# Kernel optimization log

Measured on AMD Instinct MI355X. Metric: run time of the kernel, lower is better.

The kernel has to match this reference:

```python
import jax, jax.numpy as jnp
import numpy as np

HEADS = 8
EPS_BN = 1e-5
EPS_L2 = 1e-12


def _conv(x, w, b=None, pad=0, groups=1):
    out = jax.lax.conv_general_dilated(
        x, w, (1, 1), [(pad, pad), (pad, pad)],
        feature_group_count=groups,
        dimension_numbers=('NCHW', 'OIHW', 'NCHW'))
    if b is not None:
        out = out + b[None, :, None, None]
    return out


def _sobel_weight(in_ch):
    # Fixed (non-trainable) Sobel kernels, exactly as built in SobelConv2d.__init__
    w = np.zeros((4, in_ch, 3, 3), np.float32)
    for idx in range(4):
        if idx % 2 == 0:
            w[idx, :, 0, :] = -1; w[idx, :, 0, 1] = -2
            w[idx, :, -1, :] = 1; w[idx, :, -1, 1] = 2
        else:
            w[idx, :, :, 0] = -1; w[idx, :, 1, 0] = -2
            w[idx, :, :, -1] = 1; w[idx, :, 1, -1] = 2
    return jnp.asarray(w)


def _l2norm(t):
    # F.normalize(p=2, dim=-1): x / clamp_min(||x||, eps)
    n = jnp.linalg.norm(t, axis=-1, keepdims=True)
    return t / jnp.maximum(n, EPS_L2)


def _forward(x_in, SAR_img, Wq, Wk, Wv, rescale, Wp, bp, pe1_w, pe2_w,
             conv3_w, conv3_b, bn_g, bn_b, sobel_b,
             conv2_w, conv2_b, conv32_w, conv32_b, dconv_w, dconv_b):
    b, h, w, c = x_in.shape
    d = c // HEADS
    n = h * w

    # --- SAR-guided mask (SARGuidedMechanism.forward) ---
    a = _conv(SAR_img, conv3_w, conv3_b, pad=1)
    # BatchNorm2d in training mode: batch statistics over (N,H,W)
    mu = a.mean(axis=(0, 2, 3), keepdims=True)
    var = a.var(axis=(0, 2, 3), keepdims=True)
    bn = (a - mu) / jnp.sqrt(var + EPS_BN) * bn_g[None, :, None, None] + bn_b[None, :, None, None]
    s = _conv(bn, _sobel_weight(SAR_img.shape[1]), sobel_b, pad=1)  # [b,4,H,W]
    sob = jnp.stack([jnp.sqrt(s[:, 0] ** 2 + s[:, 1] ** 2),
                     jnp.sqrt(s[:, 2] ** 2 + s[:, 3] ** 2)], axis=1)  # [b,2,H,W]
    sar_sobel = sob + bn
    e1 = _conv(sar_sobel, conv2_w, conv2_b)                           # 1x1 conv -> [b,c,H,W]
    e2 = jax.nn.sigmoid(_conv(sar_sobel, conv32_w, conv32_b, pad=1))
    e3 = _conv(e1, dconv_w, dconv_b, pad=2, groups=c)                 # depth_conv(conv2(.)) == depthwise(e1)
    mask = (e1 + e2 + e3).transpose(0, 2, 3, 1).reshape(b, n, c)      # [b,n,c]

    # --- channel (transposed) attention ---
    x = x_in.reshape(b, n, c)
    q_inp = x @ Wq
    k_inp = x @ Wk
    v_inp = x @ Wv

    def split(t):  # [b,n,(heads d)] -> [b,heads,d,n]
        return t.reshape(b, n, HEADS, d).transpose(0, 2, 3, 1)

    q = _l2norm(split(q_inp))          # normalize over token axis n
    k = _l2norm(split(k_inp))
    v = split(v_inp * mask)            # SAR gate fused into V

    attn = jnp.einsum('bhin,bhjn->bhij', k, q) * rescale[None]        # [b,heads,d,d]
    attn = jax.nn.softmax(attn, axis=-1)
    o = jnp.einsum('bhij,bhjn->bhin', attn, v)                        # [b,heads,d,n]
    o = o.transpose(0, 3, 1, 2).reshape(b, n, c)
    out_c = (o @ Wp + bp).reshape(b, h, w, c)

    # --- positional branch: depthwise conv -> GELU -> depthwise conv on v_inp ---
    vim = v_inp.reshape(b, h, w, c).transpose(0, 3, 1, 2)
    pe = _conv(vim, pe1_w, pad=1, groups=c)
    pe = jax.nn.gelu(pe, approximate=False)
    pe = _conv(pe, pe2_w, pad=1, groups=c).transpose(0, 2, 3, 1)

    return out_c + pe


def setup_inputs() -> dict:
    key = jax.random.key(0)
    ks = jax.random.split(key, 12)
    b, H, W, C, CS = 1, 256, 256, 512, 2
    wgt = lambda k, shp, sc=0.05: jax.random.normal(k, shp, jnp.float32) * sc
    return {
        'x_in': jax.random.normal(ks[0], (b, H, W, C), jnp.float32),
        'SAR_img': jax.random.normal(ks[1], (b, CS, H, W), jnp.float32),
        'Wq': wgt(ks[2], (C, C)),
        'Wk': wgt(ks[3], (C, C)),
        'Wv': wgt(ks[4], (C, C)),
        'rescale': jnp.ones((HEADS, 1, 1), jnp.float32),
        'Wp': wgt(ks[5], (C, C)),
        'bp': jnp.zeros((C,), jnp.float32),
        'pe1_w': wgt(ks[6], (C, 1, 3, 3), 0.1),
        'pe2_w': wgt(ks[7], (C, 1, 3, 3), 0.1),
        'conv3_w': wgt(ks[8], (CS, CS, 3, 3), 0.2),
        'conv3_b': jnp.zeros((CS,), jnp.float32),
        'bn_g': jnp.ones((CS,), jnp.float32),
        'bn_b': jnp.zeros((CS,), jnp.float32),
        'sobel_b': jnp.zeros((4,), jnp.float32),
        'conv2_w': wgt(ks[9], (C, CS, 1, 1), 0.1),
        'conv2_b': jnp.zeros((C,), jnp.float32),
        'conv32_w': wgt(ks[10], (C, CS, 3, 3), 0.1),
        'conv32_b': jnp.zeros((C,), jnp.float32),
        'dconv_w': wgt(ks[11], (C, 1, 5, 5), 0.1),
        'dconv_b': jnp.zeros((C,), jnp.float32),
    }


def reference(x_in, SAR_img, Wq, Wk, Wv, rescale, Wp, bp, pe1_w, pe2_w,
              conv3_w, conv3_b, bn_g, bn_b, sobel_b,
              conv2_w, conv2_b, conv32_w, conv32_b, dconv_w, dconv_b):
    return _forward(x_in, SAR_img, Wq, Wk, Wv, rescale, Wp, bp, pe1_w, pe2_w,
                    conv3_w, conv3_b, bn_g, bn_b, sobel_b,
                    conv2_w, conv2_b, conv32_w, conv32_b, dconv_w, dconv_b)
```

## Files before the change

### kernel.cpp

```cpp
#include <hip/hip_runtime.h>
#include <cstdint>
#include <cstdio>

typedef unsigned short u16;
typedef __attribute__((ext_vector_type(8))) short short8;
typedef __attribute__((ext_vector_type(4))) float f32x4;

#define DEVFN __device__ __forceinline__

DEVFN u16 f2bf(float f){ union{float f; unsigned u;} v; v.f=f; unsigned r = v.u + 0x7fffu + ((v.u>>16)&1u); return (u16)(r>>16); }
DEVFN float bf2f(u16 h){ union{unsigned u; float f;} v; v.u = ((unsigned)h)<<16; return v.f; }

#define GLOAD_LDS16(gp, lp) __builtin_amdgcn_global_load_lds( \
    (const __attribute__((address_space(1))) void*)(gp), \
    (__attribute__((address_space(3))) void*)(lp), 16, 0, 0)

static constexpr int NTOK = 65536;
static constexpr int GSPLIT = 32;
static constexpr int GKLEN  = NTOK / GSPLIT;

static constexpr size_t MB = 1024 * 1024;
static constexpr size_t OFF_XB    = 0;
static constexpr size_t OFF_XBT   = 64 * MB;
static constexpr size_t OFF_VB    = 128 * MB;
static constexpr size_t OFF_VT    = 192 * MB;
static constexpr size_t OFF_GPART = 256 * MB;
static constexpr size_t OFF_G     = 288 * MB;
static constexpr size_t OFF_TQ    = 289 * MB;
static constexpr size_t OFF_TK    = 290 * MB;
static constexpr size_t OFF_WVT   = 291 * MB;
static constexpr size_t OFF_W2T   = 291 * MB + 524288;
static constexpr size_t OFF_ASAR  = 292 * MB;
static constexpr size_t OFF_SS    = 292 * MB + 524288;
static constexpr size_t OFF_BNP   = 293 * MB;
static constexpr size_t OFF_QN    = 293 * MB + 4096;
static constexpr size_t OFF_KN    = 293 * MB + 8192;
static constexpr size_t OFF_ATTN  = 293 * MB + 12288;
static constexpr size_t WS_NEEDED = 294 * MB;

template<int MODE>
__global__ __launch_bounds__(256) void gemm_bt(
    const u16* __restrict__ A, int lda,
    const u16* __restrict__ B, int ldb,
    int klen,
    void* __restrict__ Cout,
    const float* __restrict__ bias)
{
  __shared__ uint4 smem[1024];
  const int tid  = threadIdx.x;
  const int lane = tid & 63;
  const int wv   = tid >> 6;
  const int wm   = (wv >> 1) * 64;
  const int wn   = (wv & 1) * 64;
  const int m0   = blockIdx.x * 128;
  const int n0   = blockIdx.y * 128;
  const int kb   = blockIdx.z * klen;

  const int q0 = tid, q1 = tid + 256;
  const size_t arow0 = (size_t)(m0 + (q0 >> 2)) * lda + (q0 & 3) * 8;
  const size_t arow1 = (size_t)(m0 + (q1 >> 2)) * lda + (q1 & 3) * 8;
  const size_t brow0 = (size_t)(n0 + (q0 >> 2)) * ldb + (q0 & 3) * 8;
  const size_t brow1 = (size_t)(n0 + (q1 >> 2)) * ldb + (q1 & 3) * 8;

  f32x4 acc[4][4] = {};
  const char* lAc = (const char*)smem;
  const char* lBc = (const char*)(smem + 512);
  const int ko = (lane >> 4) * 16;
  const int ma = lane & 15;

  for (int k0 = kb; k0 < kb + klen; k0 += 32) {
    __syncthreads();
    GLOAD_LDS16(&A[arow0 + k0], &smem[q0]);
    GLOAD_LDS16(&A[arow1 + k0], &smem[q1]);
    GLOAD_LDS16(&B[brow0 + k0], &smem[512 + q0]);
    GLOAD_LDS16(&B[brow1 + k0], &smem[512 + q1]);
    __syncthreads();
    short8 af[4], bfr[4];
#pragma unroll
    for (int mt = 0; mt < 4; mt++)
      af[mt] = *(const short8*)(lAc + (wm + mt * 16 + ma) * 64 + ko);
#pragma unroll
    for (int nt = 0; nt < 4; nt++)
      bfr[nt] = *(const short8*)(lBc + (wn + nt * 16 + ma) * 64 + ko);
#pragma unroll
    for (int mt = 0; mt < 4; mt++)
#pragma unroll
      for (int nt = 0; nt < 4; nt++)
        acc[mt][nt] = __builtin_amdgcn_mfma_f32_16x16x32_bf16(af[mt], bfr[nt], acc[mt][nt], 0, 0, 0);
  }

  const int col = lane & 15;
  const int rq  = (lane >> 4) * 4;
  float* Cf = (float*)Cout;
  u16*   Ch = (u16*)Cout;
  if (MODE == 1) Cf += (size_t)blockIdx.z * 512 * 512;
#pragma unroll
  for (int mt = 0; mt < 4; mt++) {
#pragma unroll
    for (int nt = 0; nt < 4; nt++) {
      const int mbase = m0 + wm + mt * 16 + rq;
      const int nn    = n0 + wn + nt * 16 + col;
#pragma unroll
      for (int r = 0; r < 4; r++) {
        float vv = acc[mt][nt][r];
        size_t idx = (size_t)(mbase + r) * 512 + nn;
        if (MODE == 0)      Ch[idx] = f2bf(vv);
        else if (MODE == 1) Cf[idx] = vv;
        else                Cf[idx] = vv + bias[nn];
      }
    }
  }
}

__global__ void k_cast_transpose(const float* __restrict__ x, u16* __restrict__ xb, u16* __restrict__ xbT)
{
  __shared__ u16 tile[64][72];
  const int t0 = blockIdx.x * 64, c0 = blockIdx.y * 64;
  const int tx = threadIdx.x & 15, ty = threadIdx.x >> 4;
#pragma unroll
  for (int p = 0; p < 4; p++) {
    int t = ty + p * 16;
    float4 v = *(const float4*)&x[(size_t)(t0 + t) * 512 + c0 + tx * 4];
    ushort4 u; u.x = f2bf(v.x); u.y = f2bf(v.y); u.z = f2bf(v.z); u.w = f2bf(v.w);
    *(ushort4*)&xb[(size_t)(t0 + t) * 512 + c0 + tx * 4] = u;
    tile[t][tx*4+0] = u.x; tile[t][tx*4+1] = u.y; tile[t][tx*4+2] = u.z; tile[t][tx*4+3] = u.w;
  }
  __syncthreads();
#pragma unroll
  for (int p = 0; p < 4; p++) {
    int c = ty + p * 16;
    ushort4 u;
    u.x = tile[tx*4+0][c]; u.y = tile[tx*4+1][c]; u.z = tile[tx*4+2][c]; u.w = tile[tx*4+3][c];
    *(ushort4*)&xbT[(size_t)(c0 + c) * 65536 + t0 + tx * 4] = u;
  }
}

__global__ void k_tbf16(const u16* __restrict__ src, u16* __restrict__ dst, int srows, int scols)
{
  __shared__ u16 tile[64][72];
  const int r0 = blockIdx.x * 64, c0v = blockIdx.y * 64;
  const int tx = threadIdx.x & 15, ty = threadIdx.x >> 4;
#pragma unroll
  for (int p = 0; p < 4; p++) {
    int r = ty + p * 16;
    ushort4 u = *(const ushort4*)&src[(size_t)(r0 + r) * scols + c0v + tx * 4];
    tile[r][tx*4+0] = u.x; tile[r][tx*4+1] = u.y; tile[r][tx*4+2] = u.z; tile[r][tx*4+3] = u.w;
  }
  __syncthreads();
#pragma unroll
  for (int p = 0; p < 4; p++) {
    int c = ty + p * 16;
    ushort4 u;
    u.x = tile[tx*4+0][c]; u.y = tile[tx*4+1][c]; u.z = tile[tx*4+2][c]; u.w = tile[tx*4+3][c];
    *(ushort4*)&dst[(size_t)(c0v + c) * srows + r0 + tx * 4] = u;
  }
}

__global__ void k_transpose_w(const float* __restrict__ Wsrc, u16* __restrict__ WT)
{
  __shared__ u16 tile[64][72];
  const int k0 = blockIdx.x * 64, n0 = blockIdx.y * 64;
  const int tx = threadIdx.x & 15, ty = threadIdx.x >> 4;
#pragma unroll
  for (int p = 0; p < 4; p++) {
    int t = ty + p * 16;
    float4 v = *(const float4*)&Wsrc[(size_t)(k0 + t) * 512 + n0 + tx * 4];
    tile[t][tx*4+0] = f2bf(v.x); tile[t][tx*4+1] = f2bf(v.y);
    tile[t][tx*4+2] = f2bf(v.z); tile[t][tx*4+3] = f2bf(v.w);
  }
  __syncthreads();
#pragma unroll
  for (int p = 0; p < 4; p++) {
    int c = ty + p * 16;
    ushort4 u;
    u.x = tile[tx*4+0][c]; u.y = tile[tx*4+1][c]; u.z = tile[tx*4+2][c]; u.w = tile[tx*4+3][c];
    *(ushort4*)&WT[(size_t)(n0 + c) * 512 + k0 + tx * 4] = u;
  }
}

__global__ void k_reduce_g(const float* __restrict__ part, float* __restrict__ G)
{
  const int i = blockIdx.x * 256 + threadIdx.x;
  float s = 0.f;
  for (int z = 0; z < GSPLIT; z++) s += part[(size_t)z * 262144 + i];
  G[i] = s;
}

__global__ __launch_bounds__(256) void k_gw(const float* __restrict__ G,
    const float* __restrict__ Wq, const float* __restrict__ Wk,
    float* __restrict__ Tq, float* __restrict__ Tk)
{
  const float* Bm = blockIdx.z ? Wk : Wq;
  float* Cm = blockIdx.z ? Tk : Tq;
  __shared__ float As[64][68];
  __shared__ float Bs[64][68];
  const int i0 = blockIdx.x * 64, j0 = blockIdx.y * 64;
  const int tx = threadIdx.x & 15, ty = threadIdx.x >> 4;
  float acc[4][4] = {};
  for (int k0 = 0; k0 < 512; k0 += 64) {
    __syncthreads();
#pragma unroll
    for (int p = 0; p < 4; p++) {
      int r = ty + p * 16;
      float4 a = *(const float4*)&G [(size_t)(i0 + r) * 512 + k0 + tx * 4];
      float4 b = *(const float4*)&Bm[(size_t)(k0 + r) * 512 + j0 + tx * 4];
      *(float4*)&As[r][tx * 4] = a;
      *(float4*)&Bs[r][tx * 4] = b;
    }
    __syncthreads();
    for (int kk = 0; kk < 64; kk++) {
      float a0 = As[ty*4+0][kk], a1 = As[ty*4+1][kk], a2 = As[ty*4+2][kk], a3 = As[ty*4+3][kk];
      float4 bq = *(const float4*)&Bs[kk][tx * 4];
      acc[0][0] += a0*bq.x; acc[0][1] += a0*bq.y; acc[0][2] += a0*bq.z; acc[0][3] += a0*bq.w;
      acc[1][0] += a1*bq.x; acc[1][1] += a1*bq.y; acc[1][2] += a1*bq.z; acc[1][3] += a1*bq.w;
      acc[2][0] += a2*bq.x; acc[2][1] += a2*bq.y; acc[2][2] += a2*bq.z; acc[2][3] += a2*bq.w;
      acc[3][0] += a3*bq.x; acc[3][1] += a3*bq.y; acc[3][2] += a3*bq.z; acc[3][3] += a3*bq.w;
    }
  }
#pragma unroll
  for (int u = 0; u < 4; u++) {
    float4 o = make_float4(acc[u][0], acc[u][1], acc[u][2], acc[u][3]);
    *(float4*)&Cm[(size_t)(i0 + ty * 4 + u) * 512 + j0 + tx * 4] = o;
  }
}

__global__ void k_norms(const float* __restrict__ Wq, const float* __restrict__ Tq,
                        const float* __restrict__ Wk, const float* __restrict__ Tk,
                        float* __restrict__ qn, float* __restrict__ kn)
{
  const int gw = (blockIdx.x * 256 + threadIdx.x) >> 6;
  const int lane = threadIdx.x & 63;
  const float* Wm = (gw < 512) ? Wq : Wk;
  const float* Tm = (gw < 512) ? Tq : Tk;
  const int c = gw & 511;
  float s = 0.f;
  for (int r = lane; r < 512; r += 64) s += Wm[(size_t)r * 512 + c] * Tm[(size_t)r * 512 + c];
  for (int off = 32; off > 0; off >>= 1) s += __shfl_down(s, off);
  if (lane == 0) {
    float n = sqrtf(fmaxf(s, 0.f));
    ((gw < 512) ? qn : kn)[c] = fmaxf(n, 1e-12f);
  }
}

__global__ __launch_bounds__(256) void k_attn(const float* __restrict__ Wk, const float* __restrict__ Tq,
    const float* __restrict__ qn, const float* __restrict__ kn,
    const float* __restrict__ rescale, float* __restrict__ attn)
{
  const int h = blockIdx.x, hd = h * 64;
  __shared__ float Ks[64][68];
  __shared__ float Qs[64][68];
  __shared__ float Ss[64][65];
  const int tx = threadIdx.x & 15, ty = threadIdx.x >> 4;
  float acc[4][4] = {};
  for (int k0 = 0; k0 < 512; k0 += 64) {
    __syncthreads();
#pragma unroll
    for (int p = 0; p < 4; p++) {
      int r = ty + p * 16;
      float4 a = *(const float4*)&Wk[(size_t)(k0 + r) * 512 + hd + tx * 4];
      float4 b = *(const float4*)&Tq[(size_t)(k0 + r) * 512 + hd + tx * 4];
      *(float4*)&Ks[r][tx * 4] = a;
      *(float4*)&Qs[r][tx * 4] = b;
    }
    __syncthreads();
    for (int kk = 0; kk < 64; kk++) {
      float a0 = Ks[kk][ty*4+0], a1 = Ks[kk][ty*4+1], a2 = Ks[kk][ty*4+2], a3 = Ks[kk][ty*4+3];
      float4 bq = *(const float4*)&Qs[kk][tx * 4];
      acc[0][0] += a0*bq.x; acc[0][1] += a0*bq.y; acc[0][2] += a0*bq.z; acc[0][3] += a0*bq.w;
      acc[1][0] += a1*bq.x; acc[1][1] += a1*bq.y; acc[1][2] += a1*bq.z; acc[1][3] += a1*bq.w;
      acc[2][0] += a2*bq.x; acc[2][1] += a2*bq.y; acc[2][2] += a2*bq.z; acc[2][3] += a2*bq.w;
      acc[3][0] += a3*bq.x; acc[3][1] += a3*bq.y; acc[3][2] += a3*bq.z; acc[3][3] += a3*bq.w;
    }
  }
#pragma unroll
  for (int u = 0; u < 4; u++)
#pragma unroll
    for (int v = 0; v < 4; v++)
      Ss[ty * 4 + u][tx * 4 + v] = acc[u][v];
  __syncthreads();
  if (threadIdx.x < 64) {
    const int i = threadIdx.x;
    const float sci = rescale[h] / kn[hd + i];
    float mx = -1e30f;
    for (int j = 0; j < 64; j++) {
      float L = Ss[i][j] * sci / qn[hd + j];
      Ss[i][j] = L;
      mx = fmaxf(mx, L);
    }
    float sum = 0.f;
    for (int j = 0; j < 64; j++) { float e = __expf(Ss[i][j] - mx); Ss[i][j] = e; sum += e; }
    float inv = 1.f / sum;
    for (int j = 0; j < 64; j++) attn[(size_t)h * 4096 + i * 64 + j] = Ss[i][j] * inv;
  }
}

__global__ void k_w2t(const float* __restrict__ attn, const float* __restrict__ Wp, u16* __restrict__ W2T)
{
  const int h = blockIdx.x >> 3, e0 = (blockIdx.x & 7) * 64;
  __shared__ float As[64][65];
  for (int p = 0; p < 16; p++) {
    int idx = p * 256 + threadIdx.x;
    As[idx >> 6][idx & 63] = attn[(size_t)h * 4096 + idx];
  }
  __syncthreads();
  const int e = e0 + (threadIdx.x & 63);
  const int j4 = threadIdx.x >> 6;
  float s[16];
#pragma unroll
  for (int jj = 0; jj < 16; jj++) s[jj] = 0.f;
  for (int i = 0; i < 64; i++) {
    float wv_ = Wp[(size_t)(h * 64 + i) * 512 + e];
#pragma unroll
    for (int jj = 0; jj < 16; jj++) s[jj] += As[i][j4 * 16 + jj] * wv_;
  }
#pragma unroll
  for (int jj = 0; jj < 16; jj++)
    W2T[(size_t)e * 512 + h * 64 + j4 * 16 + jj] = f2bf(s[jj]);
}

__global__ void k_conv3(const float* __restrict__ sar, const float* __restrict__ w3,
                        const float* __restrict__ b3, float* __restrict__ a)
{
  const int oc = blockIdx.y;
  const int p = blockIdx.x * 256 + threadIdx.x;
  const int y = p >> 8, x = p & 255;
  float s = b3[oc];
#pragma unroll
  for (int ic = 0; ic < 2; ic++) {
    const float* img = sar + ic * 65536;
    const float* w = w3 + oc * 18 + ic * 9;
#pragma unroll
    for (int k = 0; k < 9; k++) {
      int yy = y + k / 3 - 1, xx = x + k % 3 - 1;
      if ((unsigned)yy < 256u && (unsigned)xx < 256u) s += w[k] * img[yy * 256 + xx];
    }
  }
  a[oc * 65536 + p] = s;
}

__global__ void k_bnstats(const float* __restrict__ a, const float* __restrict__ g,
                          const float* __restrict__ b, float* __restrict__ bnp)
{
  const int ch = blockIdx.x;
  const int tid = threadIdx.x;
  const float* src = a + ch * 65536;
  float s = 0.f, sq = 0.f;
  for (int i = tid; i < 65536; i += 256) { float v = src[i]; s += v; sq += v * v; }
  __shared__ float rs[256], rq[256];
  rs[tid] = s; rq[tid] = sq;
  __syncthreads();
  for (int o = 128; o > 0; o >>= 1) {
    if (tid < o) { rs[tid] += rs[tid + o]; rq[tid] += rq[tid + o]; }
    __syncthreads();
  }
  if (tid == 0) {
    float mu = rs[0] * (1.f / 65536.f);
    float var = rq[0] * (1.f / 65536.f) - mu * mu;
    float scale = g[ch] / sqrtf(var + 1e-5f);
    bnp[ch] = scale;
    bnp[2 + ch] = b[ch] - mu * scale;
  }
}

__global__ void k_sar2(const float* __restrict__ a, const float* __restrict__ bnp,
                       const float* __restrict__ sb, float* __restrict__ ss)
{
  const int p = blockIdx.x * 256 + threadIdx.x;
  const int y = p >> 8, x = p & 255;
  const float sc0 = bnp[0], sc1 = bnp[1], sh0 = bnp[2], sh1 = bnp[3];
  float bs[9];
  float bn0c = 0.f, bn1c = 0.f;
#pragma unroll
  for (int k = 0; k < 9; k++) {
    int yy = y + k / 3 - 1, xx = x + k % 3 - 1;
    float v0 = 0.f, v1 = 0.f;
    if ((unsigned)yy < 256u && (unsigned)xx < 256u) {
      int q = yy * 256 + xx;
      v0 = a[q] * sc0 + sh0;
      v1 = a[65536 + q] * sc1 + sh1;
    }
    bs[k] = v0 + v1;
    if (k == 4) { bn0c = v0; bn1c = v1; }
  }
  float gv = (bs[6] + 2.f * bs[7] + bs[8]) - (bs[0] + 2.f * bs[1] + bs[2]);
  float gh = (bs[2] + 2.f * bs[5] + bs[8]) - (bs[0] + 2.f * bs[3] + bs[6]);
  float s0 = gv + sb[0], s1 = gh + sb[1], s2 = gv + sb[2], s3 = gh + sb[3];
  ss[p]         = sqrtf(s0 * s0 + s1 * s1) + bn0c;
  ss[65536 + p] = sqrtf(s2 * s2 + s3 * s3) + bn1c;
}

__global__ __launch_bounds__(256) void k_mask2(
    const float* __restrict__ ss,
    const float* __restrict__ w2,  const float* __restrict__ b2,
    const float* __restrict__ w32, const float* __restrict__ b32,
    const float* __restrict__ dw,  const float* __restrict__ db,
    const u16* __restrict__ vt, u16* __restrict__ vmt)
{
  __shared__ __align__(16) float sw0[1296];
  __shared__ __align__(16) float sw1[1296];
  __shared__ __align__(16) float swi[1296];
  const int bxx = blockIdx.x & 7, byy = blockIdx.x >> 3;
  const int tx0 = bxx * 32, ty0 = byy * 32;
  const int c0 = blockIdx.y * 4;
  const bool border = (bxx == 0) || (bxx == 7) || (byy == 0) || (byy == 7);

  for (int i = threadIdx.x; i < 1296; i += 256) {
    int r = i / 36, cl = i - r * 36;
    int gy = ty0 - 2 + r, gx = tx0 - 2 + cl;
    bool in = ((unsigned)gy < 256u) & ((unsigned)gx < 256u);
    int gp = gy * 256 + gx;
    sw0[i] = in ? ss[gp] : 0.f;
    sw1[i] = in ? ss[65536 + gp] : 0.f;
    swi[i] = in ? 1.f : 0.f;
  }
  __syncthreads();

  const int g = threadIdx.x & 7;
  const int row = threadIdx.x >> 3;
  float u0[4][4] = {}, u1[4][4] = {}, ui[4][4] = {}, a32[4][4] = {};
  float s0c[4], s1c[4];

#pragma unroll
  for (int ky = 0; ky < 5; ky++) {
    const float* rp0 = &sw0[(row + ky) * 36 + g * 4];
    const float* rp1 = &sw1[(row + ky) * 36 + g * 4];
    float4 p0a = *(const float4*)rp0, p0b = *(const float4*)(rp0 + 4);
    float4 p1a = *(const float4*)rp1, p1b = *(const float4*)(rp1 + 4);
    float r0[8] = {p0a.x, p0a.y, p0a.z, p0a.w, p0b.x, p0b.y, p0b.z, p0b.w};
    float r1[8] = {p1a.x, p1a.y, p1a.z, p1a.w, p1b.x, p1b.y, p1b.z, p1b.w};
    if (ky == 2) {
#pragma unroll
      for (int j = 0; j < 4; j++) { s0c[j] = r0[j + 2]; s1c[j] = r1[j + 2]; }
    }
#pragma unroll
    for (int dx = 0; dx < 5; dx++) {
#pragma unroll
      for (int cc = 0; cc < 4; cc++) {
        float wdw = dw[(c0 + cc) * 25 + ky * 5 + dx];
#pragma unroll
        for (int j = 0; j < 4; j++) {
          u0[cc][j] += wdw * r0[dx + j];
          u1[cc][j] += wdw * r1[dx + j];
        }
      }
    }
    if (border) {
      const float* rpi = &swi[(row + ky) * 36 + g * 4];
      float4 pia = *(const float4*)rpi, pib = *(const float4*)(rpi + 4);
      float ri[8] = {pia.x, pia.y, pia.z, pia.w, pib.x, pib.y, pib.z, pib.w};
#pragma unroll
      for (int dx = 0; dx < 5; dx++)
#pragma unroll
        for (int cc = 0; cc < 4; cc++) {
          float wdw = dw[(c0 + cc) * 25 + ky * 5 + dx];
#pragma unroll
          for (int j = 0; j < 4; j++) ui[cc][j] += wdw * ri[dx + j];
        }
    }
    if (ky >= 1 && ky <= 3) {
#pragma unroll
      for (int dx = 0; dx < 3; dx++)
#pragma unroll
        for (int cc = 0; cc < 4; cc++) {
          float wa = w32[(c0 + cc) * 18 + (ky - 1) * 3 + dx];
          float wb = w32[(c0 + cc) * 18 + 9 + (ky - 1) * 3 + dx];
#pragma unroll
          for (int j = 0; j < 4; j++)
            a32[cc][j] += wa * r0[dx + 1 + j] + wb * r1[dx + 1 + j];
        }
    }
  }

  const int y = ty0 + row, xg = tx0 + g * 4;
#pragma unroll
  for (int cc = 0; cc < 4; cc++) {
    const int c = c0 + cc;
    const float a = w2[c * 2], b = w2[c * 2 + 1], beta = b2[c];
    const float bb = b32[c], dbv = db[c];
    float wsum = 0.f;
    if (!border) {
#pragma unroll
      for (int t = 0; t < 25; t++) wsum += dw[c * 25 + t];
    }
    ushort4 vv = *(const ushort4*)&vt[(size_t)c * 65536 + y * 256 + xg];
    float vf[4] = {bf2f(vv.x), bf2f(vv.y), bf2f(vv.z), bf2f(vv.w)};
    ushort4 o;
    u16 ov[4];
#pragma unroll
    for (int j = 0; j < 4; j++) {
      float W = border ? ui[cc][j] : wsum;
      float sig = 1.f / (1.f + __expf(-(a32[cc][j] + bb)));
      float m = a * (s0c[j] + u0[cc][j]) + b * (s1c[j] + u1[cc][j])
              + beta * (1.f + W) + sig + dbv;
      ov[j] = f2bf(vf[j] * m);
    }
    o.x = ov[0]; o.y = ov[1]; o.z = ov[2]; o.w = ov[3];
    *(ushort4*)&vmt[(size_t)c * 65536 + y * 256 + xg] = o;
  }
}

DEVFN void dw3x3_row4(const u16* plane, int y, int x0, int sub,
                      const float* w9, float& s0, float& s1, float& s2, float& s3)
{
#pragma unroll
  for (int r = 0; r < 3; r++) {
    int yy = y + r - 1;
    if ((unsigned)yy < 256u) {
      const int base = yy * 256 + x0 + sub * 4;
      ushort4 p = *(const ushort4*)&plane[base];
      float v0 = bf2f(p.x), v1 = bf2f(p.y), v2 = bf2f(p.z), v3 = bf2f(p.w);
      float lf = __shfl_up(v3, 1);
      float rt = __shfl_down(v0, 1);
      if (sub == 0)  lf = (x0 > 0)   ? bf2f(plane[yy * 256 + x0 - 1])  : 0.f;
      if (sub == 15) rt = (x0 < 192) ? bf2f(plane[yy * 256 + x0 + 64]) : 0.f;
      const float wa = w9[r * 3], wb = w9[r * 3 + 1], wc = w9[r * 3 + 2];
      s0 += wa * lf + wb * v0 + wc * v1;
      s1 += wa * v0 + wb * v1 + wc * v2;
      s2 += wa * v1 + wb * v2 + wc * v3;
      s3 += wa * v2 + wb * v3 + wc * rt;
    }
  }
}

__global__ __launch_bounds__(256) void k_pe1v(const u16* __restrict__ vt,
    const float* __restrict__ w, u16* __restrict__ gt)
{
  const int t = blockIdx.x;
  const int y = t >> 2, x0 = (t & 3) * 64;
  const int cg = blockIdx.y * 64;
  const int lane = threadIdx.x & 63, wvq = threadIdx.x >> 6;
  const int sub = lane & 15, chq = lane >> 4;
#pragma unroll
  for (int i = 0; i < 4; i++) {
    const int c = cg + wvq * 16 + i * 4 + chq;
    const u16* plane = vt + (size_t)c * 65536;
    float w9[9];
#pragma unroll
    for (int k = 0; k < 9; k++) w9[k] = w[c * 9 + k];
    float s0 = 0.f, s1 = 0.f, s2 = 0.f, s3 = 0.f;
    dw3x3_row4(plane, y, x0, sub, w9, s0, s1, s2, s3);
    const float ksc = 0.70710678118654752f;
    s0 = 0.5f * s0 * (1.f + erff(s0 * ksc));
    s1 = 0.5f * s1 * (1.f + erff(s1 * ksc));
    s2 = 0.5f * s2 * (1.f + erff(s2 * ksc));
    s3 = 0.5f * s3 * (1.f + erff(s3 * ksc));
    ushort4 o; o.x = f2bf(s0); o.y = f2bf(s1); o.z = f2bf(s2); o.w = f2bf(s3);
    *(ushort4*)&gt[(size_t)c * 65536 + y * 256 + x0 + sub * 4] = o;
  }
}

__global__ __launch_bounds__(256) void k_pe2v(const u16* __restrict__ gt,
    const float* __restrict__ w, float* __restrict__ out)
{
  __shared__ float tile[64][65];
  const int t = blockIdx.x;
  const int y = t >> 2, x0 = (t & 3) * 64;
  const int cg = blockIdx.y * 64;
  const int lane = threadIdx.x & 63, wvq = threadIdx.x >> 6;
  const int sub = lane & 15, chq = lane >> 4;
#pragma unroll
  for (int i = 0; i < 4; i++) {
    const int cl = wvq * 16 + i * 4 + chq;
    const int c = cg + cl;
    const u16* plane = gt + (size_t)c * 65536;
    float w9[9];
#pragma unroll
    for (int k = 0; k < 9; k++) w9[k] = w[c * 9 + k];
    float s0 = 0.f, s1 = 0.f, s2 = 0.f, s3 = 0.f;
    dw3x3_row4(plane, y, x0, sub, w9, s0, s1, s2, s3);
    tile[cl][sub * 4 + 0] = s0;
    tile[cl][sub * 4 + 1] = s1;
    tile[cl][sub * 4 + 2] = s2;
    tile[cl][sub * 4 + 3] = s3;
  }
  __syncthreads();
#pragma unroll
  for (int k = 0; k < 4; k++) {
    const int idx = k * 256 + threadIdx.x;
    const int q = idx & 15, pl = idx >> 4;
    float4 add = make_float4(tile[q * 4 + 0][pl], tile[q * 4 + 1][pl],
                             tile[q * 4 + 2][pl], tile[q * 4 + 3][pl]);
    float* op = &out[(size_t)(y * 256 + x0 + pl) * 512 + cg + q * 4];
    float4 o = *(float4*)op;
    o.x += add.x; o.y += add.y; o.z += add.z; o.w += add.w;
    *(float4*)op = o;
  }
}

extern "C" void kernel_launch(void* const* d_in, const int* in_sizes, int n_in,
                              void* d_out, int out_size, void* d_ws, size_t ws_size,
                              hipStream_t stream)
{
  (void)in_sizes; (void)n_in; (void)out_size;
  const float* x    = (const float*)d_in[0];
  const float* sar  = (const float*)d_in[1];
  const float* Wq   = (const float*)d_in[2];
  const float* Wk   = (const float*)d_in[3];
  const float* Wv   = (const float*)d_in[4];
  const float* resc = (const float*)d_in[5];
  const float* Wp   = (const float*)d_in[6];
  const float* bp   = (const float*)d_in[7];
  const float* pe1w = (const float*)d_in[8];
  const float* pe2w = (const float*)d_in[9];
  const float* w3   = (const float*)d_in[10];
  const float* b3   = (const float*)d_in[11];
  const float* bng  = (const float*)d_in[12];
  const float* bnb  = (const float*)d_in[13];
  const float* sb   = (const float*)d_in[14];
  const float* w2c  = (const float*)d_in[15];
  const float* b2c  = (const float*)d_in[16];
  const float* w32  = (const float*)d_in[17];
  const float* b32  = (const float*)d_in[18];
  const float* dw   = (const float*)d_in[19];
  const float* db   = (const float*)d_in[20];
  float* out = (float*)d_out;

  if (ws_size < WS_NEEDED)
    fprintf(stderr, "MS_MSA: workspace too small: have %zu need %zu\n", ws_size, WS_NEEDED);

  char* ws = (char*)d_ws;
  u16* XB    = (u16*)(ws + OFF_XB);
  u16* XBT   = (u16*)(ws + OFF_XBT);
  u16* VB    = (u16*)(ws + OFF_VB);
  u16* VT    = (u16*)(ws + OFF_VT);
  float* GPART = (float*)(ws + OFF_GPART);
  float* G     = (float*)(ws + OFF_G);
  float* TQ    = (float*)(ws + OFF_TQ);
  float* TK    = (float*)(ws + OFF_TK);
  u16* WVT   = (u16*)(ws + OFF_WVT);
  u16* W2T   = (u16*)(ws + OFF_W2T);
  float* ASAR = (float*)(ws + OFF_ASAR);
  float* SS   = (float*)(ws + OFF_SS);
  float* BNP  = (float*)(ws + OFF_BNP);
  float* QN   = (float*)(ws + OFF_QN);
  float* KN   = (float*)(ws + OFF_KN);
  float* ATTN = (float*)(ws + OFF_ATTN);
  u16* VMT = XB;
  u16* GT  = XBT;
  u16* VM  = VB;

  k_cast_transpose<<<dim3(1024, 8), 256, 0, stream>>>(x, XB, XBT);
  gemm_bt<1><<<dim3(4, 4, GSPLIT), 256, 0, stream>>>(XBT, NTOK, XBT, NTOK, GKLEN, GPART, nullptr);
  k_reduce_g<<<1024, 256, 0, stream>>>(GPART, G);
  k_transpose_w<<<dim3(8, 8), 256, 0, stream>>>(Wv, WVT);
  gemm_bt<0><<<dim3(512, 4), 256, 0, stream>>>(XB, 512, WVT, 512, 512, VB, nullptr);
  k_tbf16<<<dim3(1024, 8), 256, 0, stream>>>(VB, VT, 65536, 512);
  k_gw<<<dim3(8, 8, 2), 256, 0, stream>>>(G, Wq, Wk, TQ, TK);
  k_norms<<<256, 256, 0, stream>>>(Wq, TQ, Wk, TK, QN, KN);
  k_attn<<<8, 256, 0, stream>>>(Wk, TQ, QN, KN, resc, ATTN);
  k_w2t<<<64, 256, 0, stream>>>(ATTN, Wp, W2T);
  k_conv3<<<dim3(256, 2), 256, 0, stream>>>(sar, w3, b3, ASAR);
  k_bnstats<<<2, 256, 0, stream>>>(ASAR, bng, bnb, BNP);
  k_sar2<<<256, 256, 0, stream>>>(ASAR, BNP, sb, SS);
  k_mask2<<<dim3(64, 128), 256, 0, stream>>>(SS, w2c, b2c, w32, b32, dw, db, VT, VMT);
  k_tbf16<<<dim3(8, 1024), 256, 0, stream>>>(VMT, VM, 512, 65536);
  gemm_bt<2><<<dim3(512, 4), 256, 0, stream>>>(VM, 512, W2T, 512, 512, out, bp);
  k_pe1v<<<dim3(1024, 8), 256, 0, stream>>>(VT, pe1w, GT);
  k_pe2v<<<dim3(1024, 8), 256, 0, stream>>>(GT, pe2w, out);
}
```

Baseline: 977.4 us.

## Recast SAR mask convolutions as bf16 split-precision MFMA GEMM over im2col patches

```diff
diff --git a/kernel.cpp b/kernel.cpp
--- a/kernel.cpp
+++ b/kernel.cpp
@@ -36,6 +36,8 @@
 static constexpr size_t OFF_QN    = 293 * MB + 4096;
 static constexpr size_t OFF_KN    = 293 * MB + 8192;
 static constexpr size_t OFF_ATTN  = 293 * MB + 12288;
+static constexpr size_t OFF_BM    = 293 * MB + 262144;
+static constexpr size_t OFF_TB    = 293 * MB + 786432;
 static constexpr size_t WS_NEEDED = 294 * MB;
 
 template<int MODE>
@@ -389,113 +391,196 @@
   ss[65536 + p] = sqrtf(s2 * s2 + s3 * s3) + bn1c;
 }
 
-__global__ __launch_bounds__(256) void k_mask2(
-    const float* __restrict__ ss,
-    const float* __restrict__ w2,  const float* __restrict__ b2,
-    const float* __restrict__ w32, const float* __restrict__ b32,
-    const float* __restrict__ dw,  const float* __restrict__ db,
-    const u16* __restrict__ vt, u16* __restrict__ vmt)
-{
-  __shared__ __align__(16) float sw0[1296];
-  __shared__ __align__(16) float sw1[1296];
-  __shared__ __align__(16) float swi[1296];
-  const int bxx = blockIdx.x & 7, byy = blockIdx.x >> 3;
-  const int tx0 = bxx * 32, ty0 = byy * 32;
-  const int c0 = blockIdx.y * 4;
-  const bool border = (bxx == 0) || (bxx == 7) || (byy == 0) || (byy == 7);
-
-  for (int i = threadIdx.x; i < 1296; i += 256) {
-    int r = i / 36, cl = i - r * 36;
-    int gy = ty0 - 2 + r, gx = tx0 - 2 + cl;
-    bool in = ((unsigned)gy < 256u) & ((unsigned)gx < 256u);
-    int gp = gy * 256 + gx;
-    sw0[i] = in ? ss[gp] : 0.f;
-    sw1[i] = in ? ss[65536 + gp] : 0.f;
-    swi[i] = in ? 1.f : 0.f;
+
+__global__ void k_dwprep(const float* __restrict__ dw, const float* __restrict__ db,
+                         const float* __restrict__ w2, const float* __restrict__ b2,
+                         const float* __restrict__ w32, const float* __restrict__ b32,
+                         u16* __restrict__ BM, float* __restrict__ TB)
+{
+  const int c = blockIdx.x * 256 + threadIdx.x;
+  if (c >= 512) return;
+  float d[25];
+  float wsum = 0.f;
+#pragma unroll
+  for (int t = 0; t < 25; t++) { d[t] = dw[c * 25 + t]; wsum += d[t]; }
+  const float a = w2[2 * c], b = w2[2 * c + 1], beta = b2[c];
+  const float C1 = beta * (1.f + wsum) + db[c];
+
+  u16* rL1 = BM + (size_t)((c >> 6) * 128 + (c & 63)) * 192;
+  u16* rL2 = rL1 + (size_t)64 * 192;
+
+#pragma unroll
+  for (int k = 0; k < 64; k++) {
+    float v1;
+    if (k < 25)       v1 = a * (d[k] + (k == 12 ? 1.f : 0.f));
+    else if (k < 50)  v1 = b * (d[k - 25] + (k == 37 ? 1.f : 0.f));
+    else if (k == 63) v1 = C1;
+    else              v1 = 0.f;
+    u16 h = f2bf(v1); u16 l = f2bf(v1 - bf2f(h));
+    rL1[k] = h; rL1[64 + k] = h; rL1[128 + k] = l;
+  }
+#pragma unroll
+  for (int k = 0; k < 64; k++) {
+    float v2 = 0.f;
+    if (k < 50) {
+      const int t = (k < 25) ? k : (k - 25);
+      const int dy = t / 5 - 2, dx = t % 5 - 2;
+      if (dy >= -1 && dy <= 1 && dx >= -1 && dx <= 1)
+        v2 = w32[c * 18 + ((k < 25) ? 0 : 9) + (dy + 1) * 3 + (dx + 1)];
+    }
+    if (k == 63) v2 = b32[c];
+    u16 h = f2bf(v2); u16 l = f2bf(v2 - bf2f(h));
+    rL2[k] = h; rL2[64 + k] = h; rL2[128 + k] = l;
+  }
+
+  float rs[5], cs[5];
+#pragma unroll
+  for (int i = 0; i < 5; i++) {
+    rs[i] = d[i*5] + d[i*5+1] + d[i*5+2] + d[i*5+3] + d[i*5+4];
+    cs[i] = d[i] + d[5+i] + d[10+i] + d[15+i] + d[20+i];
+  }
+  float* tb = TB + (size_t)c * 32;
+  tb[0] = rs[0];  tb[1] = rs[0] + rs[1];
+  tb[2] = rs[4];  tb[3] = rs[3] + rs[4];
+  tb[4] = cs[0];  tb[5] = cs[0] + cs[1];
+  tb[6] = cs[4];  tb[7] = cs[3] + cs[4];
+  tb[8]  = d[0];           tb[9]  = d[0] + d[1];
+  tb[10] = d[0] + d[5];    tb[11] = d[0] + d[1] + d[5] + d[6];
+  tb[12] = d[4];           tb[13] = d[3] + d[4];
+  tb[14] = d[4] + d[9];    tb[15] = d[3] + d[4] + d[8] + d[9];
+  tb[16] = d[20];          tb[17] = d[20] + d[21];
+  tb[18] = d[15] + d[20];  tb[19] = d[15] + d[16] + d[20] + d[21];
+  tb[20] = d[24];          tb[21] = d[23] + d[24];
+  tb[22] = d[19] + d[24];  tb[23] = d[18] + d[19] + d[23] + d[24];
+#pragma unroll
+  for (int i = 24; i < 32; i++) tb[i] = 0.f;
+}
+
+__global__ __launch_bounds__(256) void k_patch(const float* __restrict__ ss, u16* __restrict__ P)
+{
+  __shared__ float s0r[5][264];
+  __shared__ float s1r[5][264];
+  const int y = blockIdx.x;
+  const int tid = threadIdx.x;
+  for (int i = tid; i < 1300; i += 256) {
+    const int r = i / 260, col = i - r * 260;
+    const int yy = y + r - 2, xx = col - 2;
+    const bool in = ((unsigned)yy < 256u) & ((unsigned)xx < 256u);
+    const int gp = yy * 256 + xx;
+    s0r[r][col] = in ? ss[gp] : 0.f;
+    s1r[r][col] = in ? ss[65536 + gp] : 0.f;
   }
   __syncthreads();
-
-  const int g = threadIdx.x & 7;
-  const int row = threadIdx.x >> 3;
-  float u0[4][4] = {}, u1[4][4] = {}, ui[4][4] = {}, a32[4][4] = {};
-  float s0c[4], s1c[4];
-
-#pragma unroll
-  for (int ky = 0; ky < 5; ky++) {
-    const float* rp0 = &sw0[(row + ky) * 36 + g * 4];
-    const float* rp1 = &sw1[(row + ky) * 36 + g * 4];
-    float4 p0a = *(const float4*)rp0, p0b = *(const float4*)(rp0 + 4);
-    float4 p1a = *(const float4*)rp1, p1b = *(const float4*)(rp1 + 4);
-    float r0[8] = {p0a.x, p0a.y, p0a.z, p0a.w, p0b.x, p0b.y, p0b.z, p0b.w};
-    float r1[8] = {p1a.x, p1a.y, p1a.z, p1a.w, p1b.x, p1b.y, p1b.z, p1b.w};
-    if (ky == 2) {
-#pragma unroll
-      for (int j = 0; j < 4; j++) { s0c[j] = r0[j + 2]; s1c[j] = r1[j + 2]; }
-    }
+  const int x = tid;
+  unsigned arr32[64];
+#pragma unroll
+  for (int i = 0; i < 64; i++) arr32[i] = 0u;
+#define PUTK(k, v) arr32[(k) >> 1] |= ((unsigned)(v)) << (((k) & 1) * 16)
+#pragma unroll
+  for (int dy = 0; dy < 5; dy++)
 #pragma unroll
     for (int dx = 0; dx < 5; dx++) {
-#pragma unroll
-      for (int cc = 0; cc < 4; cc++) {
-        float wdw = dw[(c0 + cc) * 25 + ky * 5 + dx];
-#pragma unroll
-        for (int j = 0; j < 4; j++) {
-          u0[cc][j] += wdw * r0[dx + j];
-          u1[cc][j] += wdw * r1[dx + j];
+      const int t = dy * 5 + dx;
+      const float v0 = s0r[dy][x + dx];
+      const float v1 = s1r[dy][x + dx];
+      const u16 h0 = f2bf(v0); const u16 l0 = f2bf(v0 - bf2f(h0));
+      const u16 h1 = f2bf(v1); const u16 l1 = f2bf(v1 - bf2f(h1));
+      PUTK(t, h0);      PUTK(25 + t, h1);
+      PUTK(64 + t, l0); PUTK(89 + t, l1);
+    }
+  PUTK(63, 0x3F80u);
+#undef PUTK
+  unsigned* dst = (unsigned*)(P + (size_t)(y * 256 + x) * 192);
+#pragma unroll
+  for (int i = 0; i < 16; i++)
+    *(uint4*)(dst + i * 4) = *(const uint4*)(arr32 + i * 4);
+#pragma unroll
+  for (int i = 0; i < 8; i++)
+    *(uint4*)(dst + 64 + i * 4) = *(const uint4*)(arr32 + i * 4);
+}
+
+__global__ __launch_bounds__(256) void k_maskmm(
+    const u16* __restrict__ P, const u16* __restrict__ BM,
+    const float* __restrict__ TB, const float* __restrict__ beta_p,
+    u16* __restrict__ VB)
+{
+  __shared__ uint4 smem[1024];
+  const int tid  = threadIdx.x;
+  const int lane = tid & 63;
+  const int wv   = tid >> 6;
+  const int m0   = blockIdx.x * 128;
+  const int g    = blockIdx.y;
+
+  const int q0 = tid, q1 = tid + 256;
+  const size_t arow0 = (size_t)(m0 + (q0 >> 2)) * 192 + (q0 & 3) * 8;
+  const size_t arow1 = (size_t)(m0 + (q1 >> 2)) * 192 + (q1 & 3) * 8;
+  const size_t brow0 = (size_t)(g * 128 + (q0 >> 2)) * 192 + (q0 & 3) * 8;
+  const size_t brow1 = (size_t)(g * 128 + (q1 >> 2)) * 192 + (q1 & 3) * 8;
+
+  f32x4 acc[2][8] = {};
+  const char* lAc = (const char*)smem;
+  const char* lBc = (const char*)(smem + 512);
+  const int ko = (lane >> 4) * 16;
+  const int ma = lane & 15;
+
+  for (int k0 = 0; k0 < 192; k0 += 32) {
+    __syncthreads();
+    GLOAD_LDS16(&P[arow0 + k0],  &smem[q0]);
+    GLOAD_LDS16(&P[arow1 + k0],  &smem[q1]);
+    GLOAD_LDS16(&BM[brow0 + k0], &smem[512 + q0]);
+    GLOAD_LDS16(&BM[brow1 + k0], &smem[512 + q1]);
+    __syncthreads();
+    short8 af[2], bfr[8];
+#pragma unroll
+    for (int mt = 0; mt < 2; mt++)
+      af[mt] = *(const short8*)(lAc + (wv * 32 + mt * 16 + ma) * 64 + ko);
+#pragma unroll
+    for (int nt = 0; nt < 8; nt++)
+      bfr[nt] = *(const short8*)(lBc + (nt * 16 + ma) * 64 + ko);
+#pragma unroll
+    for (int mt = 0; mt < 2; mt++)
+#pragma unroll
+      for (int nt = 0; nt < 8; nt++)
+        acc[mt][nt] = __builtin_amdgcn_mfma_f32_16x16x32_bf16(af[mt], bfr[nt], acc[mt][nt], 0, 0, 0);
+  }
+
+  const int col = lane & 15, rq = (lane >> 4) * 4;
+  const int y   = m0 >> 8;
+  const int mty = (y < 2) ? (2 - y) : 0;
+  const int mby = (y > 253) ? (y - 253) : 0;
+#pragma unroll
+  for (int mt = 0; mt < 2; mt++) {
+#pragma unroll
+    for (int nt = 0; nt < 4; nt++) {
+      const int ch = g * 64 + nt * 16 + col;
+#pragma unroll
+      for (int r = 0; r < 4; r++) {
+        const int px = m0 + wv * 32 + mt * 16 + rq + r;
+        const float L1 = acc[mt][nt][r];
+        const float L2 = acc[mt][nt + 4][r];
+        const int x  = px & 255;
+        const int ml = (x < 2) ? (2 - x) : 0;
+        const int mr = (x > 253) ? (x - 253) : 0;
+        float wc = 0.f;
+        if (mty | mby | ml | mr) {
+          const float* tb = &TB[(size_t)ch * 32];
+          float W = 0.f;
+          if (mty) W -= tb[mty - 1];
+          if (mby) W -= tb[2 + mby - 1];
+          if (ml)  W -= tb[4 + ml - 1];
+          if (mr)  W -= tb[6 + mr - 1];
+          if (mty && ml) W += tb[8  + (mty - 1) * 2 + (ml - 1)];
+          if (mty && mr) W += tb[12 + (mty - 1) * 2 + (mr - 1)];
+          if (mby && ml) W += tb[16 + (mby - 1) * 2 + (ml - 1)];
+          if (mby && mr) W += tb[20 + (mby - 1) * 2 + (mr - 1)];
+          wc = beta_p[ch] * W;
         }
+        const float sig  = 1.f / (1.f + __expf(-L2));
+        const float mask = L1 + wc + sig;
+        const size_t idx = (size_t)px * 512 + ch;
+        VB[idx] = f2bf(bf2f(VB[idx]) * mask);
       }
     }
-    if (border) {
-      const float* rpi = &swi[(row + ky) * 36 + g * 4];
-      float4 pia = *(const float4*)rpi, pib = *(const float4*)(rpi + 4);
-      float ri[8] = {pia.x, pia.y, pia.z, pia.w, pib.x, pib.y, pib.z, pib.w};
-#pragma unroll
-      for (int dx = 0; dx < 5; dx++)
-#pragma unroll
-        for (int cc = 0; cc < 4; cc++) {
-          float wdw = dw[(c0 + cc) * 25 + ky * 5 + dx];
-#pragma unroll
-          for (int j = 0; j < 4; j++) ui[cc][j] += wdw * ri[dx + j];
-        }
-    }
-    if (ky >= 1 && ky <= 3) {
-#pragma unroll
-      for (int dx = 0; dx < 3; dx++)
-#pragma unroll
-        for (int cc = 0; cc < 4; cc++) {
-          float wa = w32[(c0 + cc) * 18 + (ky - 1) * 3 + dx];
-          float wb = w32[(c0 + cc) * 18 + 9 + (ky - 1) * 3 + dx];
-#pragma unroll
-          for (int j = 0; j < 4; j++)
-            a32[cc][j] += wa * r0[dx + 1 + j] + wb * r1[dx + 1 + j];
-        }
-    }
-  }
-
-  const int y = ty0 + row, xg = tx0 + g * 4;
-#pragma unroll
-  for (int cc = 0; cc < 4; cc++) {
-    const int c = c0 + cc;
-    const float a = w2[c * 2], b = w2[c * 2 + 1], beta = b2[c];
-    const float bb = b32[c], dbv = db[c];
-    float wsum = 0.f;
-    if (!border) {
-#pragma unroll
-      for (int t = 0; t < 25; t++) wsum += dw[c * 25 + t];
-    }
-    ushort4 vv = *(const ushort4*)&vt[(size_t)c * 65536 + y * 256 + xg];
-    float vf[4] = {bf2f(vv.x), bf2f(vv.y), bf2f(vv.z), bf2f(vv.w)};
-    ushort4 o;
-    u16 ov[4];
-#pragma unroll
-    for (int j = 0; j < 4; j++) {
-      float W = border ? ui[cc][j] : wsum;
-      float sig = 1.f / (1.f + __expf(-(a32[cc][j] + bb)));
-      float m = a * (s0c[j] + u0[cc][j]) + b * (s1c[j] + u1[cc][j])
-              + beta * (1.f + W) + sig + dbv;
-      ov[j] = f2bf(vf[j] * m);
-    }
-    o.x = ov[0]; o.y = ov[1]; o.z = ov[2]; o.w = ov[3];
-    *(ushort4*)&vmt[(size_t)c * 65536 + y * 256 + xg] = o;
   }
 }
 
@@ -635,9 +720,10 @@
   float* QN   = (float*)(ws + OFF_QN);
   float* KN   = (float*)(ws + OFF_KN);
   float* ATTN = (float*)(ws + OFF_ATTN);
-  u16* VMT = XB;
+  u16*  BM   = (u16*)(ws + OFF_BM);
+  float* TBt  = (float*)(ws + OFF_TB);
   u16* GT  = XBT;
-  u16* VM  = VB;
+  u16* P   = (u16*)(ws + OFF_GPART);
 
   k_cast_transpose<<<dim3(1024, 8), 256, 0, stream>>>(x, XB, XBT);
   gemm_bt<1><<<dim3(4, 4, GSPLIT), 256, 0, stream>>>(XBT, NTOK, XBT, NTOK, GKLEN, GPART, nullptr);
@@ -652,9 +738,10 @@
   k_conv3<<<dim3(256, 2), 256, 0, stream>>>(sar, w3, b3, ASAR);
   k_bnstats<<<2, 256, 0, stream>>>(ASAR, bng, bnb, BNP);
   k_sar2<<<256, 256, 0, stream>>>(ASAR, BNP, sb, SS);
-  k_mask2<<<dim3(64, 128), 256, 0, stream>>>(SS, w2c, b2c, w32, b32, dw, db, VT, VMT);
-  k_tbf16<<<dim3(8, 1024), 256, 0, stream>>>(VMT, VM, 512, 65536);
-  gemm_bt<2><<<dim3(512, 4), 256, 0, stream>>>(VM, 512, W2T, 512, 512, out, bp);
+  k_dwprep<<<2, 256, 0, stream>>>(dw, db, w2c, b2c, w32, b32, BM, TBt);
+  k_patch<<<256, 256, 0, stream>>>(SS, P);
+  k_maskmm<<<dim3(512, 8), 256, 0, stream>>>(P, BM, TBt, b2c, VB);
+  gemm_bt<2><<<dim3(512, 4), 256, 0, stream>>>(VB, 512, W2T, 512, 512, out, bp);
   k_pe1v<<<dim3(1024, 8), 256, 0, stream>>>(VT, pe1w, GT);
   k_pe2v<<<dim3(1024, 8), 256, 0, stream>>>(GT, pe2w, out);
 }
```

Measured after the change: 953.2 us. -2.5%, faster.
